# Optimization experiments

Hardware: AMD Instinct MI355X
Metric: run time of the kernel (lower is better)

## Reference

```python
import jax, jax.numpy as jnp
import numpy as np

B, N, C, H = 2, 4096, 256, 4
EPS = 1e-12  # torch F.normalize eps


def setup_inputs() -> dict:
    key = jax.random.key(0)
    k1, k2, k3, k4 = jax.random.split(key, 4)
    x = jax.random.normal(k1, (B, N, C), dtype=jnp.float32)
    w_qkv = jax.random.normal(k2, (3 * C, C), dtype=jnp.float32) * (1.0 / np.sqrt(C))
    w_out = jax.random.normal(k3, (C, C), dtype=jnp.float32) * (1.0 / np.sqrt(C))
    b_out = jnp.zeros((C,), dtype=jnp.float32)
    temperature = jnp.ones((H, 1, 1), dtype=jnp.float32)
    return {"x": x, "w_qkv": w_qkv, "w_out": w_out, "b_out": b_out,
            "temperature": temperature}


def _l2norm(t):
    # torch.nn.functional.normalize(t, dim=-1): t / max(||t||_2, eps)
    n = jnp.sqrt(jnp.sum(t * t, axis=-1, keepdims=True))
    return t / jnp.maximum(n, EPS)


def reference(x, w_qkv, w_out, b_out, temperature):
    b, n, c = x.shape
    d = c // H
    qkv = x @ w_qkv.T                                   # [B,N,3C]
    qkv = qkv.reshape(b, n, 3, H, d).transpose(2, 0, 3, 1, 4)  # [3,B,H,N,d]
    q, k, v = qkv[0], qkv[1], qkv[2]                    # each [B,H,N,d]
    # transpose(-2,-1) -> [B,H,d,N]; normalize along N (per channel over tokens)
    q = _l2norm(jnp.swapaxes(q, -2, -1))                # [B,H,d,N]
    k = _l2norm(jnp.swapaxes(k, -2, -1))                # [B,H,d,N]
    v = jnp.swapaxes(v, -2, -1)                         # [B,H,d,N]
    # attn[n,m] = sum_d q[d,n] * k[d,m], scaled by learned per-head temperature
    attn = jnp.einsum('bhdn,bhdm->bhnm', q, k) * temperature  # [B,H,N,N]
    attn = jax.nn.softmax(attn, axis=-1)
    # (attn @ v^T): [B,H,N,N] @ [B,H,N,d] -> [B,H,N,d]
    out = jnp.einsum('bhnm,bhdm->bhnd', attn, v)        # [B,H,N,d]
    # faithful to source: permute(0,3,1,2) -> [B,d,H,N], then reshape(B,N,C)
    out = out.transpose(0, 3, 1, 2).reshape(b, n, c)
    return out @ w_out.T + b_out
```

## Files before the change

kernel.cpp:

```cpp
#include <hip/hip_runtime.h>

typedef _Float16 f16;
typedef f16 f16x8 __attribute__((ext_vector_type(8)));
typedef f16 f16x4 __attribute__((ext_vector_type(4)));
typedef __fp16 fp16x2 __attribute__((ext_vector_type(2)));
typedef float f32x4 __attribute__((ext_vector_type(4)));
typedef float f32x16 __attribute__((ext_vector_type(16)));
typedef unsigned int u32;

#define NTOK 4096

#define GLL(gsrc, ldst) \
  __builtin_amdgcn_global_load_lds( \
      (const __attribute__((address_space(1))) void*)(gsrc), \
      (__attribute__((address_space(3))) void*)(ldst), 16, 0, 0)

__global__ __launch_bounds__(256) void k_cvt(
    const float* __restrict__ x, const float* __restrict__ wq,
    const float* __restrict__ wo,
    f16* __restrict__ xb, f16* __restrict__ wqb, f16* __restrict__ wob)
{
  const int bx = blockIdx.x;
  const float* src; f16* dst; int off;
  if (bx < 2048)      { src = x;  dst = xb;  off = bx * 1024; }
  else if (bx < 2240) { src = wq; dst = wqb; off = (bx - 2048) * 1024; }
  else                { src = wo; dst = wob; off = (bx - 2240) * 1024; }
  const int i = off + threadIdx.x * 4;
  float4 f = *(const float4*)(src + i);
  f16x4 h;
  h[0] = (f16)f.x; h[1] = (f16)f.y; h[2] = (f16)f.z; h[3] = (f16)f.w;
  *(f16x4*)(dst + i) = h;
}

__global__ __launch_bounds__(256) void k_gemm(
    const f16* __restrict__ A, const f16* __restrict__ W,
    int K, int mode,
    f16* __restrict__ Qb, f16* __restrict__ Kb, f16* __restrict__ Vtb,
    float* __restrict__ outF, const float* __restrict__ bias,
    float* __restrict__ partQ, float* __restrict__ partK)
{
  __shared__ f16 Al[64 * 40];
  __shared__ f16 Wl[64 * 40];
  __shared__ float redl[4][64];
  const int t = threadIdx.x;
  const int w = t >> 6, l = t & 63;
  const int lrow = l & 15, lk = l >> 4;
  const int m0 = blockIdx.y * 64, nc0 = blockIdx.x * 64;
  f32x4 acc[4] = {};
  const int srow = t >> 2, sseg = t & 3;
  for (int k0 = 0; k0 < K; k0 += 32) {
    __syncthreads();
    f16x8 av = *(const f16x8*)(A + (size_t)(m0 + srow) * K + k0 + sseg * 8);
    f16x8 wv = *(const f16x8*)(W + (size_t)(nc0 + srow) * K + k0 + sseg * 8);
    *(f16x8*)(Al + srow * 40 + sseg * 8) = av;
    *(f16x8*)(Wl + srow * 40 + sseg * 8) = wv;
    __syncthreads();
    f16x8 af = *(const f16x8*)(Al + (w * 16 + lrow) * 40 + lk * 8);
#pragma unroll
    for (int ct = 0; ct < 4; ++ct) {
      f16x8 bf = *(const f16x8*)(Wl + (ct * 16 + lrow) * 40 + lk * 8);
      acc[ct] = __builtin_amdgcn_mfma_f32_16x16x32_f16(af, bf, acc[ct], 0, 0, 0);
    }
  }
  const int nb = m0 + w * 16 + lk * 4;
  if (mode == 0) {
    const int b = nb >> 12, n = nb & 4095;
#pragma unroll
    for (int ct = 0; ct < 4; ++ct) {
      int gc = nc0 + ct * 16 + lrow;
      int s = gc >> 8, h = (gc >> 6) & 3, dd = gc & 63;
      int bh = b * 4 + h;
      if (s == 2) {
        f16x4 v;
#pragma unroll
        for (int j = 0; j < 4; ++j) v[j] = (f16)acc[ct][j];
        *(f16x4*)(Vtb + ((size_t)bh * 64 + dd) * 4096 + n) = v;
      } else {
        f16* dst = (s == 0) ? Qb : Kb;
#pragma unroll
        for (int j = 0; j < 4; ++j)
          dst[((size_t)bh * 4096 + n + j) * 64 + dd] = (f16)acc[ct][j];
      }
    }
    if (nc0 < 512) {
#pragma unroll
      for (int ct = 0; ct < 4; ++ct) {
        float v = acc[ct][0] * acc[ct][0] + acc[ct][1] * acc[ct][1]
                + acc[ct][2] * acc[ct][2] + acc[ct][3] * acc[ct][3];
        v += __shfl_xor(v, 16, 64);
        v += __shfl_xor(v, 32, 64);
        if (lk == 0) redl[w][ct * 16 + lrow] = v;
      }
      __syncthreads();
      if (t < 64) {
        float sq = redl[0][t] + redl[1][t] + redl[2][t] + redl[3][t];
        const int s = nc0 >> 8, h2 = (nc0 >> 6) & 3;
        const int b2 = m0 >> 12, mb = (m0 >> 6) & 63;
        float* dst = (s == 0) ? partQ : partK;
        dst[((b2 * 4 + h2) * 64 + mb) * 64 + t] = sq;
      }
    }
  } else {
#pragma unroll
    for (int ct = 0; ct < 4; ++ct) {
      int gc = nc0 + ct * 16 + lrow;
      float bv = bias[gc];
#pragma unroll
      for (int j = 0; j < 4; ++j)
        outF[(size_t)(nb + j) * 256 + gc] = acc[ct][j] + bv;
    }
  }
}

__global__ __launch_bounds__(512) void k_norm2(
    const float* __restrict__ partQ, const float* __restrict__ partK,
    const float* __restrict__ temp, f16* __restrict__ cqh)
{
  const int t = threadIdx.x;
  const int bh = t >> 6, dd = t & 63;
  float sq = 0.f, sk = 0.f;
  for (int s = 0; s < 64; ++s) {
    sq += partQ[(bh * 64 + s) * 64 + dd];
    sk += partK[(bh * 64 + s) * 64 + dd];
  }
  float c = temp[bh & 3] * 1.4426950408889634f /
            (fmaxf(sqrtf(sq), 1e-12f) * fmaxf(sqrtf(sk), 1e-12f));
  cqh[t] = (f16)c;
}

__device__ inline void plane_swap(u32& a, u32& b) {
  asm volatile("v_permlane32_swap_b32 %0, %1" : "+v"(a), "+v"(b));
}

__global__ __launch_bounds__(512, 2) void k_flash4(
    const f16* __restrict__ Qb, const f16* __restrict__ Kb,
    const f16* __restrict__ Vtb, const f16* __restrict__ cqh,
    f16* __restrict__ Y)
{
  __shared__ f16 KVl[32768];
  __shared__ float Lsh[512];
  const int t = threadIdx.x, w = t >> 6, l = t & 63;
  const int r = l & 31, hi = l >> 5;
  const int ks = w >> 1, qh = w & 1;
  const int r7 = r & 7;
  int nb2 = (blockIdx.x & 7) * 32 + (blockIdx.x >> 3);
  const int bh = nb2 >> 5, qt = nb2 & 31;
  const size_t base = (size_t)bh * NTOK * 64;
  f16x8 qf[2][4];
  {
    const f16* cp = cqh + bh * 64;
#pragma unroll
    for (int s = 0; s < 2; ++s) {
      const f16* qp = Qb + base + (size_t)(qt * 128 + qh * 64 + s * 32 + r) * 64 + hi * 8;
#pragma unroll
      for (int c = 0; c < 4; ++c)
        qf[s][c] = *(const f16x8*)(qp + c * 16) * *(const f16x8*)(cp + c * 16 + hi * 8);
    }
  }
  const f16* srcK = Kb + base + (size_t)(w * 8 + (l >> 3)) * 64 + ((l & 7) ^ (l >> 3)) * 8;
  const int vrow = w * 4 + (l >> 4);
  const f16* srcV = Vtb + base + (size_t)vrow * 4096 + ((l & 15) ^ (vrow & 7)) * 8;
  const int dK = w * 8 * 64;
  const int dV = 8192 + w * 4 * 128;
#define STAGE(cur, tile) { \
    const f16* sk_ = srcK + (size_t)(tile) * 8192; \
    const f16* sv_ = srcV + (tile) * 128; \
    GLL(sk_,          KVl + (cur) * 16384 + dK); \
    GLL(sk_ + 4096,   KVl + (cur) * 16384 + dK + 4096); \
    GLL(sv_,          KVl + (cur) * 16384 + dV); \
    GLL(sv_ + 131072, KVl + (cur) * 16384 + dV + 4096); }
  const int kro = (ks * 32 + r) * 64;
  const int kc0 = ((0 + hi) ^ r7) * 8, kc1 = ((2 + hi) ^ r7) * 8;
  const int kc2 = ((4 + hi) ^ r7) * 8, kc3 = ((6 + hi) ^ r7) * 8;
  const int vb0 = 8192 + r * 128, vb1 = 8192 + (32 + r) * 128;
  const int vc0 = ((ks * 4 + 0 + hi) ^ r7) * 8, vc1 = ((ks * 4 + 2 + hi) ^ r7) * 8;

  f32x16 oacc[2][2] = {};
  float ls[2] = {0.f, 0.f};
  STAGE(0, 0);
  __syncthreads();
  for (int tl = 0; tl < 32; ++tl) {
    const int cur = tl & 1;
    if (tl < 31) STAGE(cur ^ 1, tl + 1);
    const f16* B = KVl + cur * 16384;
    f16x8 kf0 = *(const f16x8*)(B + kro + kc0);
    f16x8 kf1 = *(const f16x8*)(B + kro + kc1);
    f16x8 kf2 = *(const f16x8*)(B + kro + kc2);
    f16x8 kf3 = *(const f16x8*)(B + kro + kc3);
    f16x8 vf00 = *(const f16x8*)(B + vb0 + vc0);
    f16x8 vf01 = *(const f16x8*)(B + vb0 + vc1);
    f16x8 vf10 = *(const f16x8*)(B + vb1 + vc0);
    f16x8 vf11 = *(const f16x8*)(B + vb1 + vc1);
#pragma unroll
    for (int s = 0; s < 2; ++s) {
      f32x16 sacc = {};
      sacc = __builtin_amdgcn_mfma_f32_32x32x16_f16(kf0, qf[s][0], sacc, 0, 0, 0);
      sacc = __builtin_amdgcn_mfma_f32_32x32x16_f16(kf1, qf[s][1], sacc, 0, 0, 0);
      sacc = __builtin_amdgcn_mfma_f32_32x32x16_f16(kf2, qf[s][2], sacc, 0, 0, 0);
      sacc = __builtin_amdgcn_mfma_f32_32x32x16_f16(kf3, qf[s][3], sacc, 0, 0, 0);
      u32 Dw[8];
#pragma unroll
      for (int u = 0; u < 4; ++u) {
#pragma unroll
        for (int v = 0; v < 2; ++v) {
          float a  = exp2f(sacc[u * 4 + v * 2]);
          float b2 = exp2f(sacc[u * 4 + v * 2 + 1]);
          ls[s] += a + b2;
          union { fp16x2 h; u32 u; } cv;
          cv.h = __builtin_amdgcn_cvt_pkrtz(a, b2);
          Dw[u * 2 + v] = cv.u;
        }
      }
      plane_swap(Dw[0], Dw[2]);
      plane_swap(Dw[1], Dw[3]);
      plane_swap(Dw[4], Dw[6]);
      plane_swap(Dw[5], Dw[7]);
      union { f16x8 v; u32 d[4]; } p0, p1;
      p0.d[0] = Dw[0]; p0.d[1] = Dw[1]; p0.d[2] = Dw[2]; p0.d[3] = Dw[3];
      p1.d[0] = Dw[4]; p1.d[1] = Dw[5]; p1.d[2] = Dw[6]; p1.d[3] = Dw[7];
      oacc[s][0] = __builtin_amdgcn_mfma_f32_32x32x16_f16(p0.v, vf00, oacc[s][0], 0, 0, 0);
      oacc[s][0] = __builtin_amdgcn_mfma_f32_32x32x16_f16(p1.v, vf01, oacc[s][0], 0, 0, 0);
      oacc[s][1] = __builtin_amdgcn_mfma_f32_32x32x16_f16(p0.v, vf10, oacc[s][1], 0, 0, 0);
      oacc[s][1] = __builtin_amdgcn_mfma_f32_32x32x16_f16(p1.v, vf11, oacc[s][1], 0, 0, 0);
    }
    __syncthreads();
  }
#undef STAGE
  ls[0] += __shfl_xor(ls[0], 32, 64);
  ls[1] += __shfl_xor(ls[1], 32, 64);
  if (hi == 0) { Lsh[w * 64 + r] = ls[0]; Lsh[w * 64 + 32 + r] = ls[1]; }
#pragma unroll
  for (int s = 0; s < 2; ++s)
#pragma unroll
    for (int dt = 0; dt < 2; ++dt) {
      f16* orow = KVl + w * 4096 + (dt * 32 + r) * 64;
      const f32x16& oa = oacc[s][dt];
#pragma unroll
      for (int u = 0; u < 4; ++u) {
        f16x4 h4;
        h4[0] = (f16)oa[u * 4 + 0]; h4[1] = (f16)oa[u * 4 + 1];
        h4[2] = (f16)oa[u * 4 + 2]; h4[3] = (f16)oa[u * 4 + 3];
        *(f16x4*)(orow + (((s * 4 + u) ^ r7) * 8) + hi * 4) = h4;
      }
    }
  __syncthreads();
  const int s2 = w >> 2, dt2 = (w >> 1) & 1, qh2 = w & 1;
  const int b = bh >> 2, h = bh & 3;
#pragma unroll
  for (int c = 0; c < 2; ++c) {
    float accv[8] = {}, denv[8] = {};
#pragma unroll
    for (int ksl = 0; ksl < 4; ++ksl) {
      const int wp = ksl * 2 + qh2;
      f16x8 rd = *(const f16x8*)(KVl + wp * 4096 + (dt2 * 32 + r) * 64 +
                                 (((s2 * 4 + hi * 2 + c) ^ r7) * 8));
      f32x4 la = *(const f32x4*)(Lsh + wp * 64 + s2 * 32 + hi * 16 + c * 8);
      f32x4 lb = *(const f32x4*)(Lsh + wp * 64 + s2 * 32 + hi * 16 + c * 8 + 4);
#pragma unroll
      for (int j = 0; j < 4; ++j) {
        accv[j]     += (float)rd[j];
        accv[4 + j] += (float)rd[4 + j];
        denv[j]     += la[j];
        denv[4 + j] += lb[j];
      }
    }
    const int ng = qt * 128 + qh2 * 64 + s2 * 32 + hi * 16 + c * 8;
    const int np = (dt2 * 32 + r) * 64 + h * 16 + (ng >> 8);
    const int cp_ = ng & 255;
    f16x8 yv;
#pragma unroll
    for (int j = 0; j < 8; ++j) yv[j] = (f16)(accv[j] / denv[j]);
    *(f16x8*)(Y + ((size_t)b * 4096 + np) * 256 + cp_) = yv;
  }
}

extern "C" void kernel_launch(void* const* d_in, const int* in_sizes, int n_in,
                              void* d_out, int out_size, void* d_ws, size_t ws_size,
                              hipStream_t stream)
{
  const float* x     = (const float*)d_in[0];
  const float* w_qkv = (const float*)d_in[1];
  const float* w_out = (const float*)d_in[2];
  const float* b_out = (const float*)d_in[3];
  const float* temp  = (const float*)d_in[4];

  char* ws = (char*)d_ws;
  f16*   xb    = (f16*)(ws);
  f16*   wqkvb = (f16*)(ws + 4 * 1024 * 1024);
  f16*   woutb = (f16*)(ws + 4 * 1024 * 1024 + 512 * 1024);
  f16*   Qb    = (f16*)(ws + 5  * 1024 * 1024);
  f16*   Kb    = (f16*)(ws + 9  * 1024 * 1024);
  f16*   Vtb   = (f16*)(ws + 13 * 1024 * 1024);
  f16*   cqh   = (f16*)(ws + 17 * 1024 * 1024);
  float* partQ = (float*)(ws + 17 * 1024 * 1024 + 8192);
  float* partK = (float*)(ws + 17 * 1024 * 1024 + 8192 + 131072);
  f16*   Y     = (f16*)(ws + 18 * 1024 * 1024);
  float* outF  = (float*)d_out;

  k_cvt<<<2304, 256, 0, stream>>>(x, w_qkv, w_out, xb, wqkvb, woutb);
  k_gemm<<<dim3(12, 128), 256, 0, stream>>>(xb, wqkvb, 256, 0, Qb, Kb, Vtb,
                                            nullptr, nullptr, partQ, partK);
  k_norm2<<<1, 512, 0, stream>>>(partQ, partK, temp, cqh);
  k_flash4<<<256, 512, 0, stream>>>(Qb, Kb, Vtb, cqh, Y);
  k_gemm<<<dim3(4, 128), 256, 0, stream>>>(Y, woutb, 256, 1, nullptr, nullptr, nullptr,
                                           outF, b_out, nullptr, nullptr);
}
```

Baseline: 96.79 us.

## Software-pipeline QK and softmax-PV across sub-tiles with setprio in flash kernel

Restructures the flash attention inner loop so the QK^T MFMAs for one query sub-tile overlap the exp/convert/PV work of the other sub-tile. The second sub-tile's softmax-PV is deferred one iteration, with its V fragments carried in registers, and a trailing epilogue drains it. LDS fragment reads now happen before the next tile's async stage is issued, and s_setprio raises wave priority around MFMA bursts. This aims to hide exp latency behind matrix ops, at the cost of extra register pressure from the carried accumulator and V fragments.

```diff
diff --git a/kernel.cpp b/kernel.cpp
--- a/kernel.cpp
+++ b/kernel.cpp
@@ -132,7 +132,7 @@
   asm volatile("v_permlane32_swap_b32 %0, %1" : "+v"(a), "+v"(b));
 }
 
-__global__ __launch_bounds__(512, 2) void k_flash4(
+__global__ __launch_bounds__(512, 2) void k_flash5(
     const f16* __restrict__ Qb, const f16* __restrict__ Kb,
     const f16* __restrict__ Vtb, const f16* __restrict__ cqh,
     f16* __restrict__ Y)
@@ -175,60 +175,77 @@
   const int vb0 = 8192 + r * 128, vb1 = 8192 + (32 + r) * 128;
   const int vc0 = ((ks * 4 + 0 + hi) ^ r7) * 8, vc1 = ((ks * 4 + 2 + hi) ^ r7) * 8;
 
+#define QKSTEP(SACC, QS) { \
+    SACC = (f32x16){}; \
+    SACC = __builtin_amdgcn_mfma_f32_32x32x16_f16(kf0, qf[QS][0], SACC, 0, 0, 0); \
+    SACC = __builtin_amdgcn_mfma_f32_32x32x16_f16(kf1, qf[QS][1], SACC, 0, 0, 0); \
+    SACC = __builtin_amdgcn_mfma_f32_32x32x16_f16(kf2, qf[QS][2], SACC, 0, 0, 0); \
+    SACC = __builtin_amdgcn_mfma_f32_32x32x16_f16(kf3, qf[QS][3], SACC, 0, 0, 0); }
+
+#define SMPV(SACC, LS, OIDX, V0, V1, V2, V3) { \
+    u32 Dw[8]; \
+    _Pragma("unroll") \
+    for (int u = 0; u < 4; ++u) { \
+      _Pragma("unroll") \
+      for (int v = 0; v < 2; ++v) { \
+        float a  = exp2f(SACC[u * 4 + v * 2]); \
+        float b2 = exp2f(SACC[u * 4 + v * 2 + 1]); \
+        LS += a + b2; \
+        union { fp16x2 h; u32 u; } cv; \
+        cv.h = __builtin_amdgcn_cvt_pkrtz(a, b2); \
+        Dw[u * 2 + v] = cv.u; \
+      } \
+    } \
+    plane_swap(Dw[0], Dw[2]); \
+    plane_swap(Dw[1], Dw[3]); \
+    plane_swap(Dw[4], Dw[6]); \
+    plane_swap(Dw[5], Dw[7]); \
+    union { f16x8 v; u32 d[4]; } p0, p1; \
+    p0.d[0] = Dw[0]; p0.d[1] = Dw[1]; p0.d[2] = Dw[2]; p0.d[3] = Dw[3]; \
+    p1.d[0] = Dw[4]; p1.d[1] = Dw[5]; p1.d[2] = Dw[6]; p1.d[3] = Dw[7]; \
+    __builtin_amdgcn_s_setprio(1); \
+    oacc[OIDX][0] = __builtin_amdgcn_mfma_f32_32x32x16_f16(p0.v, V0, oacc[OIDX][0], 0, 0, 0); \
+    oacc[OIDX][0] = __builtin_amdgcn_mfma_f32_32x32x16_f16(p1.v, V1, oacc[OIDX][0], 0, 0, 0); \
+    oacc[OIDX][1] = __builtin_amdgcn_mfma_f32_32x32x16_f16(p0.v, V2, oacc[OIDX][1], 0, 0, 0); \
+    oacc[OIDX][1] = __builtin_amdgcn_mfma_f32_32x32x16_f16(p1.v, V3, oacc[OIDX][1], 0, 0, 0); \
+    __builtin_amdgcn_s_setprio(0); }
+
   f32x16 oacc[2][2] = {};
-  float ls[2] = {0.f, 0.f};
+  f32x16 saccA = {}, saccB = {};
+  float ls0 = 0.f, ls1 = 0.f;
+  f16x8 vfp0 = {}, vfp1 = {}, vfp2 = {}, vfp3 = {};
   STAGE(0, 0);
   __syncthreads();
   for (int tl = 0; tl < 32; ++tl) {
     const int cur = tl & 1;
+    const f16* Bb = KVl + cur * 16384;
+    f16x8 kf0 = *(const f16x8*)(Bb + kro + kc0);
+    f16x8 kf1 = *(const f16x8*)(Bb + kro + kc1);
+    f16x8 kf2 = *(const f16x8*)(Bb + kro + kc2);
+    f16x8 kf3 = *(const f16x8*)(Bb + kro + kc3);
+    f16x8 vfc0 = *(const f16x8*)(Bb + vb0 + vc0);
+    f16x8 vfc1 = *(const f16x8*)(Bb + vb0 + vc1);
+    f16x8 vfc2 = *(const f16x8*)(Bb + vb1 + vc0);
+    f16x8 vfc3 = *(const f16x8*)(Bb + vb1 + vc1);
     if (tl < 31) STAGE(cur ^ 1, tl + 1);
-    const f16* B = KVl + cur * 16384;
-    f16x8 kf0 = *(const f16x8*)(B + kro + kc0);
-    f16x8 kf1 = *(const f16x8*)(B + kro + kc1);
-    f16x8 kf2 = *(const f16x8*)(B + kro + kc2);
-    f16x8 kf3 = *(const f16x8*)(B + kro + kc3);
-    f16x8 vf00 = *(const f16x8*)(B + vb0 + vc0);
-    f16x8 vf01 = *(const f16x8*)(B + vb0 + vc1);
-    f16x8 vf10 = *(const f16x8*)(B + vb1 + vc0);
-    f16x8 vf11 = *(const f16x8*)(B + vb1 + vc1);
-#pragma unroll
-    for (int s = 0; s < 2; ++s) {
-      f32x16 sacc = {};
-      sacc = __builtin_amdgcn_mfma_f32_32x32x16_f16(kf0, qf[s][0], sacc, 0, 0, 0);
-      sacc = __builtin_amdgcn_mfma_f32_32x32x16_f16(kf1, qf[s][1], sacc, 0, 0, 0);
-      sacc = __builtin_amdgcn_mfma_f32_32x32x16_f16(kf2, qf[s][2], sacc, 0, 0, 0);
-      sacc = __builtin_amdgcn_mfma_f32_32x32x16_f16(kf3, qf[s][3], sacc, 0, 0, 0);
-      u32 Dw[8];
-#pragma unroll
-      for (int u = 0; u < 4; ++u) {
-#pragma unroll
-        for (int v = 0; v < 2; ++v) {
-          float a  = exp2f(sacc[u * 4 + v * 2]);
-          float b2 = exp2f(sacc[u * 4 + v * 2 + 1]);
-          ls[s] += a + b2;
-          union { fp16x2 h; u32 u; } cv;
-          cv.h = __builtin_amdgcn_cvt_pkrtz(a, b2);
-          Dw[u * 2 + v] = cv.u;
-        }
-      }
-      plane_swap(Dw[0], Dw[2]);
-      plane_swap(Dw[1], Dw[3]);
-      plane_swap(Dw[4], Dw[6]);
-      plane_swap(Dw[5], Dw[7]);
-      union { f16x8 v; u32 d[4]; } p0, p1;
-      p0.d[0] = Dw[0]; p0.d[1] = Dw[1]; p0.d[2] = Dw[2]; p0.d[3] = Dw[3];
-      p1.d[0] = Dw[4]; p1.d[1] = Dw[5]; p1.d[2] = Dw[6]; p1.d[3] = Dw[7];
-      oacc[s][0] = __builtin_amdgcn_mfma_f32_32x32x16_f16(p0.v, vf00, oacc[s][0], 0, 0, 0);
-      oacc[s][0] = __builtin_amdgcn_mfma_f32_32x32x16_f16(p1.v, vf01, oacc[s][0], 0, 0, 0);
-      oacc[s][1] = __builtin_amdgcn_mfma_f32_32x32x16_f16(p0.v, vf10, oacc[s][1], 0, 0, 0);
-      oacc[s][1] = __builtin_amdgcn_mfma_f32_32x32x16_f16(p1.v, vf11, oacc[s][1], 0, 0, 0);
-    }
+    __builtin_amdgcn_s_setprio(1);
+    QKSTEP(saccA, 0);
+    __builtin_amdgcn_s_setprio(0);
+    if (tl > 0) SMPV(saccB, ls1, 1, vfp0, vfp1, vfp2, vfp3);
+    __builtin_amdgcn_s_setprio(1);
+    QKSTEP(saccB, 1);
+    __builtin_amdgcn_s_setprio(0);
+    SMPV(saccA, ls0, 0, vfc0, vfc1, vfc2, vfc3);
+    vfp0 = vfc0; vfp1 = vfc1; vfp2 = vfc2; vfp3 = vfc3;
     __syncthreads();
   }
+  SMPV(saccB, ls1, 1, vfp0, vfp1, vfp2, vfp3);
 #undef STAGE
-  ls[0] += __shfl_xor(ls[0], 32, 64);
-  ls[1] += __shfl_xor(ls[1], 32, 64);
-  if (hi == 0) { Lsh[w * 64 + r] = ls[0]; Lsh[w * 64 + 32 + r] = ls[1]; }
+#undef QKSTEP
+#undef SMPV
+  ls0 += __shfl_xor(ls0, 32, 64);
+  ls1 += __shfl_xor(ls1, 32, 64);
+  if (hi == 0) { Lsh[w * 64 + r] = ls0; Lsh[w * 64 + 32 + r] = ls1; }
 #pragma unroll
   for (int s = 0; s < 2; ++s)
 #pragma unroll
@@ -301,7 +318,7 @@
   k_gemm<<<dim3(12, 128), 256, 0, stream>>>(xb, wqkvb, 256, 0, Qb, Kb, Vtb,
                                             nullptr, nullptr, partQ, partK);
   k_norm2<<<1, 512, 0, stream>>>(partQ, partK, temp, cqh);
-  k_flash4<<<256, 512, 0, stream>>>(Qb, Kb, Vtb, cqh, Y);
+  k_flash5<<<256, 512, 0, stream>>>(Qb, Kb, Vtb, cqh, Y);
   k_gemm<<<dim3(4, 128), 256, 0, stream>>>(Y, woutb, 256, 1, nullptr, nullptr, nullptr,
                                            outF, b_out, nullptr, nullptr);
 }
```

Measured after the change: 88.59 us. 8.5% less time.

## Halve flash query tile to double grid and occupancy, add MFMA priority hints

Applied to the files above, without the earlier changes.

The flash-attention kernel now handles 64 queries per block instead of 128. The grid doubles to 512 blocks, and launch bounds ask for 4 blocks per CU so that register pressure drops and more waves stay resident. It also issues the LDS fragment reads before the next tile's async prefetch, raises wave priority around the MFMA groups, and uses the raw exp2 builtin. The trade-off is that every K/V tile is now loaded from global memory twice as often across blocks. The epilogue reduction layout is reworked to fit the smaller tile.

```diff
diff --git a/kernel.cpp b/kernel.cpp
--- a/kernel.cpp
+++ b/kernel.cpp
@@ -132,30 +132,28 @@
   asm volatile("v_permlane32_swap_b32 %0, %1" : "+v"(a), "+v"(b));
 }
 
-__global__ __launch_bounds__(512, 2) void k_flash4(
+__global__ __launch_bounds__(512, 4) void k_flash6(
     const f16* __restrict__ Qb, const f16* __restrict__ Kb,
     const f16* __restrict__ Vtb, const f16* __restrict__ cqh,
     f16* __restrict__ Y)
 {
   __shared__ f16 KVl[32768];
-  __shared__ float Lsh[512];
+  __shared__ float Lsh[256];
   const int t = threadIdx.x, w = t >> 6, l = t & 63;
   const int r = l & 31, hi = l >> 5;
   const int ks = w >> 1, qh = w & 1;
   const int r7 = r & 7;
-  int nb2 = (blockIdx.x & 7) * 32 + (blockIdx.x >> 3);
-  const int bh = nb2 >> 5, qt = nb2 & 31;
+  int nb2 = (blockIdx.x & 7) * 64 + (blockIdx.x >> 3);
+  const int bh = nb2 >> 6, qt = nb2 & 63;
   const size_t base = (size_t)bh * NTOK * 64;
-  f16x8 qf[2][4];
+  f16x8 qf0, qf1, qf2, qf3;
   {
-    const f16* cp = cqh + bh * 64;
-#pragma unroll
-    for (int s = 0; s < 2; ++s) {
-      const f16* qp = Qb + base + (size_t)(qt * 128 + qh * 64 + s * 32 + r) * 64 + hi * 8;
-#pragma unroll
-      for (int c = 0; c < 4; ++c)
-        qf[s][c] = *(const f16x8*)(qp + c * 16) * *(const f16x8*)(cp + c * 16 + hi * 8);
-    }
+    const f16* cq = cqh + bh * 64;
+    const f16* qp = Qb + base + (size_t)(qt * 64 + qh * 32 + r) * 64 + hi * 8;
+    qf0 = *(const f16x8*)(qp)      * *(const f16x8*)(cq +  0 + hi * 8);
+    qf1 = *(const f16x8*)(qp + 16) * *(const f16x8*)(cq + 16 + hi * 8);
+    qf2 = *(const f16x8*)(qp + 32) * *(const f16x8*)(cq + 32 + hi * 8);
+    qf3 = *(const f16x8*)(qp + 48) * *(const f16x8*)(cq + 48 + hi * 8);
   }
   const f16* srcK = Kb + base + (size_t)(w * 8 + (l >> 3)) * 64 + ((l & 7) ^ (l >> 3)) * 8;
   const int vrow = w * 4 + (l >> 4);
@@ -175,103 +173,98 @@
   const int vb0 = 8192 + r * 128, vb1 = 8192 + (32 + r) * 128;
   const int vc0 = ((ks * 4 + 0 + hi) ^ r7) * 8, vc1 = ((ks * 4 + 2 + hi) ^ r7) * 8;
 
-  f32x16 oacc[2][2] = {};
-  float ls[2] = {0.f, 0.f};
+  f32x16 oacc0 = {}, oacc1 = {};
+  float lsw = 0.f;
   STAGE(0, 0);
   __syncthreads();
   for (int tl = 0; tl < 32; ++tl) {
     const int cur = tl & 1;
+    const f16* Bb = KVl + cur * 16384;
+    f16x8 kf0 = *(const f16x8*)(Bb + kro + kc0);
+    f16x8 kf1 = *(const f16x8*)(Bb + kro + kc1);
+    f16x8 kf2 = *(const f16x8*)(Bb + kro + kc2);
+    f16x8 kf3 = *(const f16x8*)(Bb + kro + kc3);
+    f16x8 vf0 = *(const f16x8*)(Bb + vb0 + vc0);
+    f16x8 vf1 = *(const f16x8*)(Bb + vb0 + vc1);
+    f16x8 vf2 = *(const f16x8*)(Bb + vb1 + vc0);
+    f16x8 vf3 = *(const f16x8*)(Bb + vb1 + vc1);
     if (tl < 31) STAGE(cur ^ 1, tl + 1);
-    const f16* B = KVl + cur * 16384;
-    f16x8 kf0 = *(const f16x8*)(B + kro + kc0);
-    f16x8 kf1 = *(const f16x8*)(B + kro + kc1);
-    f16x8 kf2 = *(const f16x8*)(B + kro + kc2);
-    f16x8 kf3 = *(const f16x8*)(B + kro + kc3);
-    f16x8 vf00 = *(const f16x8*)(B + vb0 + vc0);
-    f16x8 vf01 = *(const f16x8*)(B + vb0 + vc1);
-    f16x8 vf10 = *(const f16x8*)(B + vb1 + vc0);
-    f16x8 vf11 = *(const f16x8*)(B + vb1 + vc1);
-#pragma unroll
-    for (int s = 0; s < 2; ++s) {
-      f32x16 sacc = {};
-      sacc = __builtin_amdgcn_mfma_f32_32x32x16_f16(kf0, qf[s][0], sacc, 0, 0, 0);
-      sacc = __builtin_amdgcn_mfma_f32_32x32x16_f16(kf1, qf[s][1], sacc, 0, 0, 0);
-      sacc = __builtin_amdgcn_mfma_f32_32x32x16_f16(kf2, qf[s][2], sacc, 0, 0, 0);
-      sacc = __builtin_amdgcn_mfma_f32_32x32x16_f16(kf3, qf[s][3], sacc, 0, 0, 0);
-      u32 Dw[8];
-#pragma unroll
-      for (int u = 0; u < 4; ++u) {
-#pragma unroll
-        for (int v = 0; v < 2; ++v) {
-          float a  = exp2f(sacc[u * 4 + v * 2]);
-          float b2 = exp2f(sacc[u * 4 + v * 2 + 1]);
-          ls[s] += a + b2;
-          union { fp16x2 h; u32 u; } cv;
-          cv.h = __builtin_amdgcn_cvt_pkrtz(a, b2);
-          Dw[u * 2 + v] = cv.u;
-        }
+    f32x16 sacc = {};
+    __builtin_amdgcn_s_setprio(1);
+    sacc = __builtin_amdgcn_mfma_f32_32x32x16_f16(kf0, qf0, sacc, 0, 0, 0);
+    sacc = __builtin_amdgcn_mfma_f32_32x32x16_f16(kf1, qf1, sacc, 0, 0, 0);
+    sacc = __builtin_amdgcn_mfma_f32_32x32x16_f16(kf2, qf2, sacc, 0, 0, 0);
+    sacc = __builtin_amdgcn_mfma_f32_32x32x16_f16(kf3, qf3, sacc, 0, 0, 0);
+    __builtin_amdgcn_s_setprio(0);
+    u32 Dw[8];
+#pragma unroll
+    for (int u = 0; u < 4; ++u) {
+#pragma unroll
+      for (int v = 0; v < 2; ++v) {
+        float a  = __builtin_amdgcn_exp2f(sacc[u * 4 + v * 2]);
+        float b2 = __builtin_amdgcn_exp2f(sacc[u * 4 + v * 2 + 1]);
+        lsw += a + b2;
+        union { fp16x2 h; u32 u; } cv;
+        cv.h = __builtin_amdgcn_cvt_pkrtz(a, b2);
+        Dw[u * 2 + v] = cv.u;
       }
-      plane_swap(Dw[0], Dw[2]);
-      plane_swap(Dw[1], Dw[3]);
-      plane_swap(Dw[4], Dw[6]);
-      plane_swap(Dw[5], Dw[7]);
-      union { f16x8 v; u32 d[4]; } p0, p1;
-      p0.d[0] = Dw[0]; p0.d[1] = Dw[1]; p0.d[2] = Dw[2]; p0.d[3] = Dw[3];
-      p1.d[0] = Dw[4]; p1.d[1] = Dw[5]; p1.d[2] = Dw[6]; p1.d[3] = Dw[7];
-      oacc[s][0] = __builtin_amdgcn_mfma_f32_32x32x16_f16(p0.v, vf00, oacc[s][0], 0, 0, 0);
-      oacc[s][0] = __builtin_amdgcn_mfma_f32_32x32x16_f16(p1.v, vf01, oacc[s][0], 0, 0, 0);
-      oacc[s][1] = __builtin_amdgcn_mfma_f32_32x32x16_f16(p0.v, vf10, oacc[s][1], 0, 0, 0);
-      oacc[s][1] = __builtin_amdgcn_mfma_f32_32x32x16_f16(p1.v, vf11, oacc[s][1], 0, 0, 0);
-    }
+    }
+    plane_swap(Dw[0], Dw[2]);
+    plane_swap(Dw[1], Dw[3]);
+    plane_swap(Dw[4], Dw[6]);
+    plane_swap(Dw[5], Dw[7]);
+    union { f16x8 v; u32 d[4]; } p0, p1;
+    p0.d[0] = Dw[0]; p0.d[1] = Dw[1]; p0.d[2] = Dw[2]; p0.d[3] = Dw[3];
+    p1.d[0] = Dw[4]; p1.d[1] = Dw[5]; p1.d[2] = Dw[6]; p1.d[3] = Dw[7];
+    __builtin_amdgcn_s_setprio(1);
+    oacc0 = __builtin_amdgcn_mfma_f32_32x32x16_f16(p0.v, vf0, oacc0, 0, 0, 0);
+    oacc0 = __builtin_amdgcn_mfma_f32_32x32x16_f16(p1.v, vf1, oacc0, 0, 0, 0);
+    oacc1 = __builtin_amdgcn_mfma_f32_32x32x16_f16(p0.v, vf2, oacc1, 0, 0, 0);
+    oacc1 = __builtin_amdgcn_mfma_f32_32x32x16_f16(p1.v, vf3, oacc1, 0, 0, 0);
+    __builtin_amdgcn_s_setprio(0);
     __syncthreads();
   }
 #undef STAGE
-  ls[0] += __shfl_xor(ls[0], 32, 64);
-  ls[1] += __shfl_xor(ls[1], 32, 64);
-  if (hi == 0) { Lsh[w * 64 + r] = ls[0]; Lsh[w * 64 + 32 + r] = ls[1]; }
-#pragma unroll
-  for (int s = 0; s < 2; ++s)
-#pragma unroll
-    for (int dt = 0; dt < 2; ++dt) {
-      f16* orow = KVl + w * 4096 + (dt * 32 + r) * 64;
-      const f32x16& oa = oacc[s][dt];
-#pragma unroll
-      for (int u = 0; u < 4; ++u) {
-        f16x4 h4;
-        h4[0] = (f16)oa[u * 4 + 0]; h4[1] = (f16)oa[u * 4 + 1];
-        h4[2] = (f16)oa[u * 4 + 2]; h4[3] = (f16)oa[u * 4 + 3];
-        *(f16x4*)(orow + (((s * 4 + u) ^ r7) * 8) + hi * 4) = h4;
-      }
-    }
+  lsw += __shfl_xor(lsw, 32, 64);
+  if (hi == 0) Lsh[w * 32 + r] = lsw;
+#pragma unroll
+  for (int dt = 0; dt < 2; ++dt) {
+    f16* orow = KVl + w * 2048 + (dt * 32 + r) * 32;
+    const f32x16& oa = dt ? oacc1 : oacc0;
+#pragma unroll
+    for (int u = 0; u < 4; ++u) {
+      f16x4 h4;
+      h4[0] = (f16)oa[u * 4 + 0]; h4[1] = (f16)oa[u * 4 + 1];
+      h4[2] = (f16)oa[u * 4 + 2]; h4[3] = (f16)oa[u * 4 + 3];
+      *(f16x4*)(orow + ((u ^ (r & 3)) * 8) + hi * 4) = h4;
+    }
+  }
   __syncthreads();
   const int s2 = w >> 2, dt2 = (w >> 1) & 1, qh2 = w & 1;
+  const int g = s2 * 2 + hi;
   const int b = bh >> 2, h = bh & 3;
-#pragma unroll
-  for (int c = 0; c < 2; ++c) {
-    float accv[8] = {}, denv[8] = {};
-#pragma unroll
-    for (int ksl = 0; ksl < 4; ++ksl) {
-      const int wp = ksl * 2 + qh2;
-      f16x8 rd = *(const f16x8*)(KVl + wp * 4096 + (dt2 * 32 + r) * 64 +
-                                 (((s2 * 4 + hi * 2 + c) ^ r7) * 8));
-      f32x4 la = *(const f32x4*)(Lsh + wp * 64 + s2 * 32 + hi * 16 + c * 8);
-      f32x4 lb = *(const f32x4*)(Lsh + wp * 64 + s2 * 32 + hi * 16 + c * 8 + 4);
-#pragma unroll
-      for (int j = 0; j < 4; ++j) {
-        accv[j]     += (float)rd[j];
-        accv[4 + j] += (float)rd[4 + j];
-        denv[j]     += la[j];
-        denv[4 + j] += lb[j];
-      }
-    }
-    const int ng = qt * 128 + qh2 * 64 + s2 * 32 + hi * 16 + c * 8;
-    const int np = (dt2 * 32 + r) * 64 + h * 16 + (ng >> 8);
-    const int cp_ = ng & 255;
-    f16x8 yv;
-#pragma unroll
-    for (int j = 0; j < 8; ++j) yv[j] = (f16)(accv[j] / denv[j]);
-    *(f16x8*)(Y + ((size_t)b * 4096 + np) * 256 + cp_) = yv;
-  }
+  float accv[8] = {}, denv[8] = {};
+#pragma unroll
+  for (int ksl = 0; ksl < 4; ++ksl) {
+    const int wp = ksl * 2 + qh2;
+    f16x8 rd = *(const f16x8*)(KVl + wp * 2048 + (dt2 * 32 + r) * 32 + ((g ^ (r & 3)) * 8));
+    f32x4 la = *(const f32x4*)(Lsh + wp * 32 + g * 8);
+    f32x4 lb = *(const f32x4*)(Lsh + wp * 32 + g * 8 + 4);
+#pragma unroll
+    for (int j = 0; j < 4; ++j) {
+      accv[j]     += (float)rd[j];
+      accv[4 + j] += (float)rd[4 + j];
+      denv[j]     += la[j];
+      denv[4 + j] += lb[j];
+    }
+  }
+  const int ng = qt * 64 + qh2 * 32 + g * 8;
+  const int np = (dt2 * 32 + r) * 64 + h * 16 + (ng >> 8);
+  const int cp_ = ng & 255;
+  f16x8 yv;
+#pragma unroll
+  for (int j = 0; j < 8; ++j) yv[j] = (f16)(accv[j] / denv[j]);
+  *(f16x8*)(Y + ((size_t)b * 4096 + np) * 256 + cp_) = yv;
 }
 
 extern "C" void kernel_launch(void* const* d_in, const int* in_sizes, int n_in,
@@ -301,7 +294,7 @@
   k_gemm<<<dim3(12, 128), 256, 0, stream>>>(xb, wqkvb, 256, 0, Qb, Kb, Vtb,
                                             nullptr, nullptr, partQ, partK);
   k_norm2<<<1, 512, 0, stream>>>(partQ, partK, temp, cqh);
-  k_flash4<<<256, 512, 0, stream>>>(Qb, Kb, Vtb, cqh, Y);
+  k_flash6<<<512, 512, 0, stream>>>(Qb, Kb, Vtb, cqh, Y);
   k_gemm<<<dim3(4, 128), 256, 0, stream>>>(Y, woutb, 256, 1, nullptr, nullptr, nullptr,
                                            outF, b_out, nullptr, nullptr);
 }
```

New measurement: 83.27 us. 1.16x faster.
